# Optimization experiments

Measured on AMD Instinct MI355X. Metric: run time of the kernel, lower is better.

The kernel has to match this reference:

```python
import jax, jax.numpy as jnp
import numpy as np

B = 32            # decode batch (N flat tokens, q_len=1 each)
D_MODEL = 4096
H = 32            # query heads
HKV = 8           # kv heads (GQA)
HD = 128          # head dim
KVLEN = 2048      # context length per sequence
BLOCK = 256       # paged-cache block size
NBPS = KVLEN // BLOCK          # blocks per sequence = 8
NBLOCKS = B * NBPS             # 256
NSLOTS = NBLOCKS * BLOCK       # 65536
EPS = 1e-6
THETA = 10000.0
NEG = -1e30


def setup_inputs() -> dict:
    key = jax.random.key(0)
    ks = jax.random.split(key, 8)
    seqs = jax.random.normal(ks[0], (B, D_MODEL), dtype=jnp.float32)
    Wq = jax.random.normal(ks[1], (D_MODEL, H * HD), dtype=jnp.float32) * 0.02
    Wk = jax.random.normal(ks[2], (D_MODEL, HKV * HD), dtype=jnp.float32) * 0.02
    Wv = jax.random.normal(ks[3], (D_MODEL, HKV * HD), dtype=jnp.float32) * 0.02
    Wo = jax.random.normal(ks[4], (H * HD, D_MODEL), dtype=jnp.float32) * 0.02
    qn_w = jnp.ones((HD,), dtype=jnp.float32)
    kn_w = jnp.ones((HD,), dtype=jnp.float32)
    k_cache = jax.random.normal(ks[5], (NSLOTS, HKV, HD), dtype=jnp.float32) * 0.02
    v_cache = jax.random.normal(ks[6], (NSLOTS, HKV, HD), dtype=jnp.float32) * 0.02
    # decode step: each seq owns NBPS contiguous blocks; new token goes to last slot
    input_pos = jnp.full((B,), KVLEN - 1, dtype=jnp.int32)
    slot_mapping = (jnp.arange(B, dtype=jnp.int32) * NBPS * BLOCK + (KVLEN - 1)).astype(jnp.int32)
    block_tables = jnp.arange(NBLOCKS, dtype=jnp.int32).reshape(B, NBPS)
    context_lens = jnp.full((B,), KVLEN, dtype=jnp.int32)
    return {
        'seqs': seqs, 'Wq': Wq, 'Wk': Wk, 'Wv': Wv, 'Wo': Wo,
        'qn_w': qn_w, 'kn_w': kn_w, 'k_cache': k_cache, 'v_cache': v_cache,
        'input_pos': input_pos, 'slot_mapping': slot_mapping,
        'block_tables': block_tables, 'context_lens': context_lens,
    }


def _rmsnorm(x, w):
    return x * jax.lax.rsqrt(jnp.mean(x * x, axis=-1, keepdims=True) + EPS) * w


def _rope(x, pos):
    # x: [N, heads, HD], pos: [N]
    half = HD // 2
    inv = 1.0 / (THETA ** (jnp.arange(half, dtype=jnp.float32) / half))
    ang = pos.astype(jnp.float32)[:, None] * inv          # [N, half]
    cos = jnp.cos(ang)[:, None, :]
    sin = jnp.sin(ang)[:, None, :]
    x1, x2 = x[..., :half], x[..., half:]
    return jnp.concatenate([x1 * cos - x2 * sin, x2 * cos + x1 * sin], axis=-1)


def reference(seqs, Wq, Wk, Wv, Wo, qn_w, kn_w, k_cache, v_cache,
              input_pos, slot_mapping, block_tables, context_lens):
    # QKV projections (flat token layout, N = B decode tokens)
    q = (seqs @ Wq).reshape(B, H, HD)
    k = (seqs @ Wk).reshape(B, HKV, HD)
    v = (seqs @ Wv).reshape(B, HKV, HD)
    # qk-norm then RoPE
    q = _rmsnorm(q, qn_w)
    k = _rmsnorm(k, kn_w)
    q = _rope(q, input_pos)
    k = _rope(k, input_pos)
    # paged KV-cache store (slot_mapping scatter)
    kc = k_cache.at[slot_mapping].set(k)
    vc = v_cache.at[slot_mapping].set(v)
    # block-table-indexed gather: slots per sequence [B, KVLEN]
    slots = (block_tables[:, :, None] * BLOCK
             + jnp.arange(BLOCK, dtype=jnp.int32)[None, None, :]).reshape(B, -1)
    K = kc[slots]   # [B, L, HKV, HD]
    V = vc[slots]   # [B, L, HKV, HD]
    L = slots.shape[1]
    # GQA attention: group query heads over kv heads
    G = H // HKV
    qg = q.reshape(B, HKV, G, HD)
    scale = 1.0 / jnp.sqrt(jnp.float32(HD))
    scores = jnp.einsum('bkgd,blkd->bkgl', qg, K) * scale   # [B, HKV, G, L]
    valid = jnp.arange(L, dtype=jnp.int32)[None, :] < context_lens[:, None]
    scores = jnp.where(valid[:, None, None, :], scores, NEG)
    p = jax.nn.softmax(scores, axis=-1)
    out = jnp.einsum('bkgl,blkd->bkgd', p, V).reshape(B, H * HD)
    return out @ Wo
```

## Files before the change

kernel.cpp:

```cpp
#include <hip/hip_runtime.h>
#include <hip/hip_bf16.h>
#include <math.h>

#define B_     32
#define DM_    4096
#define H_     32
#define HKV_   8
#define G_     4
#define HD_    128
#define KVLEN_ 2048
#define NBPS_  8
#define NQKV_  6144
#define QKSPLIT_ 32
#define QKC_     128
#define OKSPLIT_ 32
#define OKC_     128
#define ASPLIT_ 16
#define APOS_  128

typedef float vf4 __attribute__((ext_vector_type(4)));
typedef float vf2 __attribute__((ext_vector_type(2)));

__global__ __launch_bounds__(256) void transpose32(
    const float* __restrict__ in, float* __restrict__ out) {
  __shared__ float t[32][65];
  const int tid = threadIdx.x;
  const int k0 = blockIdx.x * 64;
  #pragma unroll
  for (int it = 0; it < 8; ++it) {
    int m = it * 4 + (tid >> 6);
    int k = tid & 63;
    t[m][k] = in[(size_t)m * DM_ + k0 + k];
  }
  __syncthreads();
  #pragma unroll
  for (int it = 0; it < 8; ++it) {
    int flat = it * 256 + tid;
    out[(size_t)k0 * 32 + flat] = t[flat & 31][flat >> 5];
  }
}

__global__ __launch_bounds__(256) void qkv_gemm(
    const float* __restrict__ seqsT, const float* __restrict__ Wq,
    const float* __restrict__ Wk, const float* __restrict__ Wv,
    float* __restrict__ P1) {
  const int tid = threadIdx.x;
  const int nid = blockIdx.x % 24;
  const int kid = blockIdx.x / 24;
  const int k0 = kid * QKC_;

  const int ct = tid & 127;
  const int mh16 = __builtin_amdgcn_readfirstlane((tid >> 7) << 4);
  const int n  = nid * 256 + ct * 2;

  const float* W; int col, ldw;
  if (nid < 16)      { W = Wq; col = n;        ldw = 4096; }
  else if (nid < 20) { W = Wk; col = n - 4096; ldw = 1024; }
  else               { W = Wv; col = n - 5120; ldw = 1024; }

  float2 acc[16];
  #pragma unroll
  for (int r = 0; r < 16; ++r) acc[r] = make_float2(0.f, 0.f);

  const vf2* wp = (const vf2*)(W + (size_t)k0 * ldw + col);
  const int ldw2 = ldw >> 1;
  const vf4* ap = (const vf4*)(seqsT + (size_t)k0 * 32 + mh16);

  #pragma unroll 8
  for (int kk = 0; kk < QKC_; ++kk) {
    vf2 w = __builtin_nontemporal_load(wp + (size_t)kk * ldw2);
    vf4 a0 = ap[kk * 8 + 0];
    vf4 a1 = ap[kk * 8 + 1];
    vf4 a2 = ap[kk * 8 + 2];
    vf4 a3 = ap[kk * 8 + 3];
    #define FMA2(av, r) \
      acc[r].x = fmaf(av, w.x, acc[r].x); acc[r].y = fmaf(av, w.y, acc[r].y);
    FMA2(a0.x, 0)  FMA2(a0.y, 1)  FMA2(a0.z, 2)  FMA2(a0.w, 3)
    FMA2(a1.x, 4)  FMA2(a1.y, 5)  FMA2(a1.z, 6)  FMA2(a1.w, 7)
    FMA2(a2.x, 8)  FMA2(a2.y, 9)  FMA2(a2.z, 10) FMA2(a2.w, 11)
    FMA2(a3.x, 12) FMA2(a3.y, 13) FMA2(a3.z, 14) FMA2(a3.w, 15)
    #undef FMA2
  }

  float* o = P1 + (size_t)kid * 32 * NQKV_ + n;
  #pragma unroll
  for (int r = 0; r < 16; ++r) {
    int m = mh16 + r;
    *(float2*)(o + (size_t)m * NQKV_) = acc[r];
  }
}

__global__ __launch_bounds__(128) void reduce_norm_rope(
    const float* __restrict__ P1, const float* __restrict__ qn_w,
    const float* __restrict__ kn_w, const int* __restrict__ input_pos,
    float* __restrict__ qf, float* __restrict__ knew, float* __restrict__ vnew) {
  const int b = blockIdx.x / 48;
  const int hh = blockIdx.x % 48;
  const int tid = threadIdx.x;

  int col0, kind;
  if (hh < 32)      { kind = 0; col0 = hh * 128; }
  else if (hh < 40) { kind = 1; col0 = 4096 + (hh - 32) * 128; }
  else              { kind = 2; col0 = 5120 + (hh - 40) * 128; }

  float x = 0.f;
  const float* p = P1 + (size_t)b * NQKV_ + col0 + tid;
  #pragma unroll
  for (int s = 0; s < QKSPLIT_; ++s) x += p[(size_t)s * 32 * NQKV_];

  if (kind == 2) {
    vnew[(size_t)b * 1024 + (hh - 40) * 128 + tid] = x;
    return;
  }

  __shared__ float lds[128];
  __shared__ float wred[2];
  float ss = x * x;
  #pragma unroll
  for (int off = 32; off > 0; off >>= 1) ss += __shfl_down(ss, off);
  if ((tid & 63) == 0) wred[tid >> 6] = ss;
  __syncthreads();
  float tot = wred[0] + wred[1];
  float r = rsqrtf(tot * (1.f / 128.f) + 1e-6f);
  const float* wv = (kind == 0) ? qn_w : kn_w;
  x = x * r * wv[tid];

  lds[tid] = x;
  __syncthreads();

  if (tid < 64) {
    float pos = (float)input_pos[b];
    float inv = exp2f(-(float)tid * 0.20762050593045952f);
    float ang = pos * inv;
    float c = cosf(ang), s = sinf(ang);
    float x1 = lds[tid], x2 = lds[tid + 64];
    float o1 = x1 * c - x2 * s;
    float o2 = x2 * c + x1 * s;
    float* dst = (kind == 0) ? (qf + (size_t)b * 4096 + hh * 128)
                             : (knew + (size_t)b * 1024 + (hh - 32) * 128);
    dst[tid] = o1;
    dst[tid + 64] = o2;
  }
}

__global__ __launch_bounds__(512, 4) void attn_decode(
    const float* __restrict__ qf, const float* __restrict__ knew,
    const float* __restrict__ vnew, const float* __restrict__ kc,
    const float* __restrict__ vc, const int* __restrict__ block_tables,
    const int* __restrict__ slot_mapping, const int* __restrict__ context_lens,
    float* __restrict__ pacc, float* __restrict__ pls) {
  const int b   = blockIdx.x >> 4;
  const int sp  = blockIdx.x & 15;
  const int tid = threadIdx.x;
  const int w   = tid >> 6;
  const int lane = tid & 63;
  const int gi  = lane >> 4;
  const int l16 = lane & 15;
  const int d0  = l16 * 8;

  const int ctx   = context_lens[b];
  const int fslot = slot_mapping[b];
  const int base  = sp * APOS_;

  const int page  = block_tables[b * NBPS_ + (base >> 8)];
  const int slot0 = (page << 8) + (base & 255);
  const int rel   = fslot - slot0;
  const bool hasf = (rel >= 0) && (rel < APOS_);
  const int nv    = min(APOS_, ctx - base);

  const float scale = 0.08838834764831845f;
  float q[4][8];
  #pragma unroll
  for (int g = 0; g < 4; ++g) {
    const float4* qp = (const float4*)(qf + ((size_t)b * H_ + w * G_ + g) * HD_ + d0);
    float4 a = qp[0], c = qp[1];
    q[g][0] = a.x * scale; q[g][1] = a.y * scale; q[g][2] = a.z * scale; q[g][3] = a.w * scale;
    q[g][4] = c.x * scale; q[g][5] = c.y * scale; q[g][6] = c.z * scale; q[g][7] = c.w * scale;
  }

  const float* knp = knew + ((size_t)b * HKV_ + w) * HD_ + d0;
  const float* vnp = vnew + ((size_t)b * HKV_ + w) * HD_ + d0;
  const float* kcb = kc + ((size_t)slot0 * HKV_ + w) * HD_ + d0;
  const float* vcb = vc + ((size_t)slot0 * HKV_ + w) * HD_ + d0;

  float ls[4] = {0.f, 0.f, 0.f, 0.f};
  float acc[4][8];
  #pragma unroll
  for (int g = 0; g < 4; ++g)
    #pragma unroll
    for (int j = 0; j < 8; ++j) acc[g][j] = 0.f;

  #define ATTN_STEP(K1, K2, V1, V2, SGN)                                  \
    {                                                                     \
      float kk8[8] = {K1.x, K1.y, K1.z, K1.w, K2.x, K2.y, K2.z, K2.w};    \
      float vv[8]  = {V1.x, V1.y, V1.z, V1.w, V2.x, V2.y, V2.z, V2.w};    \
      float s[4];                                                         \
      _Pragma("unroll")                                                   \
      for (int g = 0; g < 4; ++g) {                                       \
        float t = 0.f;                                                    \
        _Pragma("unroll")                                                 \
        for (int j = 0; j < 8; ++j) t = fmaf(q[g][j], kk8[j], t);         \
        s[g] = t;                                                         \
      }                                                                   \
      _Pragma("unroll")                                                   \
      for (int o2 = 1; o2 < 16; o2 <<= 1) {                               \
        _Pragma("unroll")                                                 \
        for (int g = 0; g < 4; ++g) s[g] += __shfl_xor(s[g], o2);         \
      }                                                                   \
      _Pragma("unroll")                                                   \
      for (int g = 0; g < 4; ++g) {                                       \
        float pw = (SGN) * __expf(s[g]);                                  \
        ls[g] += pw;                                                      \
        _Pragma("unroll")                                                 \
        for (int j = 0; j < 8; ++j) acc[g][j] = fmaf(pw, vv[j], acc[g][j]); \
      }                                                                   \
    }

  if (nv == APOS_) {
    #pragma unroll 2
    for (int it = 0; it < APOS_ / 4; ++it) {
      const int off = it * 4 + gi;
      const vf4* kp4 = (const vf4*)(kcb + (size_t)off * (HKV_ * HD_));
      const vf4* vp4 = (const vf4*)(vcb + (size_t)off * (HKV_ * HD_));
      vf4 k1 = __builtin_nontemporal_load(kp4);
      vf4 k2 = __builtin_nontemporal_load(kp4 + 1);
      vf4 v1 = __builtin_nontemporal_load(vp4);
      vf4 v2 = __builtin_nontemporal_load(vp4 + 1);
      ATTN_STEP(k1, k2, v1, v2, 1.f)
    }
    if (hasf && gi == (rel & 3)) {
      const float* kps = kcb + (size_t)rel * (HKV_ * HD_);
      const float* vps = vcb + (size_t)rel * (HKV_ * HD_);
      float4 k1 = ((const float4*)kps)[0];
      float4 k2 = ((const float4*)kps)[1];
      float4 v1 = ((const float4*)vps)[0];
      float4 v2 = ((const float4*)vps)[1];
      ATTN_STEP(k1, k2, v1, v2, -1.f)
      float4 f1 = ((const float4*)knp)[0];
      float4 f2 = ((const float4*)knp)[1];
      float4 g1 = ((const float4*)vnp)[0];
      float4 g2 = ((const float4*)vnp)[1];
      ATTN_STEP(f1, f2, g1, g2, 1.f)
    }
  } else {
    for (int it = 0; it < APOS_ / 4; ++it) {
      const int off = it * 4 + gi;
      if (base + off < ctx) {
        const float* kp = (off == rel) ? knp : (kcb + (size_t)off * (HKV_ * HD_));
        const float* vp = (off == rel) ? vnp : (vcb + (size_t)off * (HKV_ * HD_));
        float4 k1 = ((const float4*)kp)[0];
        float4 k2 = ((const float4*)kp)[1];
        float4 v1 = ((const float4*)vp)[0];
        float4 v2 = ((const float4*)vp)[1];
        ATTN_STEP(k1, k2, v1, v2, 1.f)
      }
    }
  }
  #undef ATTN_STEP

  #pragma unroll
  for (int o2 = 16; o2 < 64; o2 <<= 1) {
    #pragma unroll
    for (int g = 0; g < 4; ++g) {
      ls[g] += __shfl_xor(ls[g], o2);
      #pragma unroll
      for (int j = 0; j < 8; ++j) acc[g][j] += __shfl_xor(acc[g][j], o2);
    }
  }

  if (gi == 0) {
    #pragma unroll
    for (int g = 0; g < 4; ++g) {
      float* dst = pacc + (((size_t)sp * B_ + b) * H_ + (w * G_ + g)) * HD_ + d0;
      float4 o1 = {acc[g][0], acc[g][1], acc[g][2], acc[g][3]};
      float4 o2 = {acc[g][4], acc[g][5], acc[g][6], acc[g][7]};
      ((float4*)dst)[0] = o1;
      ((float4*)dst)[1] = o2;
      if (l16 == 0) pls[((size_t)sp * B_ + b) * H_ + (w * G_ + g)] = ls[g];
    }
  }
}

__global__ __launch_bounds__(256) void attn_mergeT(
    const float* __restrict__ pacc, const float* __restrict__ pls,
    float* __restrict__ attnT) {
  const int idx = blockIdx.x * 256 + threadIdx.x;
  const int b   = idx >> 10;
  const int h   = (idx >> 5) & 31;
  const int d4  = (idx & 31) * 4;
  const int bh  = idx >> 5;
  const float4* p4 = (const float4*)pacc;
  float4 A = {0.f, 0.f, 0.f, 0.f};
  float L = 0.f;
  #pragma unroll
  for (int sp = 0; sp < ASPLIT_; ++sp) {
    float4 t = p4[(size_t)sp * 32768 + idx];
    A.x += t.x; A.y += t.y; A.z += t.z; A.w += t.w;
    L += pls[sp * (B_ * H_) + bh];
  }
  float r = 1.f / L;
  float* dst = attnT + ((size_t)(h * 128 + d4)) * 32 + b;
  dst[0]  = A.x * r;
  dst[32] = A.y * r;
  dst[64] = A.z * r;
  dst[96] = A.w * r;
}

__global__ __launch_bounds__(256) void oproj_gemm(
    const float* __restrict__ attnT, const float* __restrict__ Wo,
    float* __restrict__ P2) {
  const int tid = threadIdx.x;
  const int nid = blockIdx.x & 15;
  const int kid = blockIdx.x >> 4;
  const int k0 = kid * OKC_;

  const int ct = tid & 127;
  const int mh16 = __builtin_amdgcn_readfirstlane((tid >> 7) << 4);
  const int n  = nid * 256 + ct * 2;

  float2 acc[16];
  #pragma unroll
  for (int r = 0; r < 16; ++r) acc[r] = make_float2(0.f, 0.f);

  const vf2* wp = (const vf2*)(Wo + (size_t)k0 * 4096 + n);
  const vf4* ap = (const vf4*)(attnT + (size_t)k0 * 32 + mh16);

  #pragma unroll 8
  for (int kk = 0; kk < OKC_; ++kk) {
    vf2 w = __builtin_nontemporal_load(wp + (size_t)kk * 2048);
    vf4 a0 = ap[kk * 8 + 0];
    vf4 a1 = ap[kk * 8 + 1];
    vf4 a2 = ap[kk * 8 + 2];
    vf4 a3 = ap[kk * 8 + 3];
    #define FMA2(av, r) \
      acc[r].x = fmaf(av, w.x, acc[r].x); acc[r].y = fmaf(av, w.y, acc[r].y);
    FMA2(a0.x, 0)  FMA2(a0.y, 1)  FMA2(a0.z, 2)  FMA2(a0.w, 3)
    FMA2(a1.x, 4)  FMA2(a1.y, 5)  FMA2(a1.z, 6)  FMA2(a1.w, 7)
    FMA2(a2.x, 8)  FMA2(a2.y, 9)  FMA2(a2.z, 10) FMA2(a2.w, 11)
    FMA2(a3.x, 12) FMA2(a3.y, 13) FMA2(a3.z, 14) FMA2(a3.w, 15)
    #undef FMA2
  }

  float* o = P2 + (size_t)kid * 32 * 4096 + n;
  #pragma unroll
  for (int r = 0; r < 16; ++r) {
    int m = mh16 + r;
    *(float2*)(o + (size_t)m * 4096) = acc[r];
  }
}

__global__ __launch_bounds__(256) void oproj_reduce(
    const float* __restrict__ P2, float* __restrict__ out) {
  const int idx = blockIdx.x * 256 + threadIdx.x;
  const float4* p4 = (const float4*)P2;
  float4 s = {0.f, 0.f, 0.f, 0.f};
  #pragma unroll
  for (int t = 0; t < OKSPLIT_; ++t) {
    float4 v = p4[(size_t)t * 32768 + idx];
    s.x += v.x; s.y += v.y; s.z += v.z; s.w += v.w;
  }
  ((float4*)out)[idx] = s;
}

extern "C" void kernel_launch(void* const* d_in, const int* in_sizes, int n_in,
                              void* d_out, int out_size, void* d_ws, size_t ws_size,
                              hipStream_t stream) {
  const float* seqs = (const float*)d_in[0];
  const float* Wq   = (const float*)d_in[1];
  const float* Wk   = (const float*)d_in[2];
  const float* Wv   = (const float*)d_in[3];
  const float* Wo   = (const float*)d_in[4];
  const float* qn_w = (const float*)d_in[5];
  const float* kn_w = (const float*)d_in[6];
  const float* kc   = (const float*)d_in[7];
  const float* vc   = (const float*)d_in[8];
  const int* input_pos = (const int*)d_in[9];
  const int* slot_map  = (const int*)d_in[10];
  const int* btab      = (const int*)d_in[11];
  const int* ctx       = (const int*)d_in[12];
  float* out = (float*)d_out;

  char* w = (char*)d_ws;
  float* seqsT = (float*)(w);
  float* P1    = (float*)(w + 524288);
  float* qf    = (float*)(w + 25690112);
  float* knew  = (float*)(w + 26214400);
  float* vnew  = (float*)(w + 26345472);
  float* attnT = (float*)(w + 26476544);
  float* pacc  = (float*)(w + 27000832);
  float* pls   = (float*)(w + 35389440);
  float* P2    = (float*)(w + 35454976);

  transpose32<<<64, 256, 0, stream>>>(seqs, seqsT);
  qkv_gemm<<<24 * QKSPLIT_, 256, 0, stream>>>(seqsT, Wq, Wk, Wv, P1);
  reduce_norm_rope<<<B_ * 48, 128, 0, stream>>>(P1, qn_w, kn_w, input_pos, qf, knew, vnew);
  attn_decode<<<B_ * ASPLIT_, 512, 0, stream>>>(qf, knew, vnew, kc, vc, btab, slot_map, ctx, pacc, pls);
  attn_mergeT<<<128, 256, 0, stream>>>(pacc, pls, attnT);
  oproj_gemm<<<16 * OKSPLIT_, 256, 0, stream>>>(attnT, Wo, P2);
  oproj_reduce<<<128, 256, 0, stream>>>(P2, out);
}
```

Before: 186.8 us.

## Stage KV cache through LDS with double-buffered global_load_lds in attention

The full-block path of the decode attention kernel now loads K and V through direct global-to-LDS loads into a per-wave double buffer. The next iteration's tile is prefetched while the current one is read from LDS, with explicit vmcnt waits. The goal is to hide memory latency and keep more loads in flight than the previous register nontemporal loads did. In exchange it uses 64KB of shared memory per block, which may limit occupancy under launch_bounds(512,4), and it adds an LDS round trip. The loop is also no longer unrolled.

```diff
diff --git a/kernel.cpp b/kernel.cpp
--- a/kernel.cpp
+++ b/kernel.cpp
@@ -21,6 +21,12 @@
 typedef float vf4 __attribute__((ext_vector_type(4)));
 typedef float vf2 __attribute__((ext_vector_type(2)));
 
+__device__ __forceinline__ void gl_lds(const float* g, float* l) {
+  __builtin_amdgcn_global_load_lds(
+      (const __attribute__((address_space(1))) void*)g,
+      (__attribute__((address_space(3))) void*)l, 16, 0, 0);
+}
+
 __global__ __launch_bounds__(256) void transpose32(
     const float* __restrict__ in, float* __restrict__ out) {
   __shared__ float t[32][65];
@@ -149,6 +155,7 @@
     const float* __restrict__ vc, const int* __restrict__ block_tables,
     const int* __restrict__ slot_mapping, const int* __restrict__ context_lens,
     float* __restrict__ pacc, float* __restrict__ pls) {
+  __shared__ float alds[16384];
   const int b   = blockIdx.x >> 4;
   const int sp  = blockIdx.x & 15;
   const int tid = threadIdx.x;
@@ -182,6 +189,12 @@
   const float* vnp = vnew + ((size_t)b * HKV_ + w) * HD_ + d0;
   const float* kcb = kc + ((size_t)slot0 * HKV_ + w) * HD_ + d0;
   const float* vcb = vc + ((size_t)slot0 * HKV_ + w) * HD_ + d0;
+
+  const float* ksrc0 = kc + (size_t)slot0 * 1024 + (size_t)(lane >> 5) * 1024
+                          + w * 128 + (lane & 31) * 4;
+  const float* vsrc0 = vc + (size_t)slot0 * 1024 + (size_t)(lane >> 5) * 1024
+                          + w * 128 + (lane & 31) * 4;
+  const int wofs = __builtin_amdgcn_readfirstlane(w * 2048);
 
   float ls[4] = {0.f, 0.f, 0.f, 0.f};
   float acc[4][8];
@@ -217,17 +230,35 @@
     }
 
   if (nv == APOS_) {
-    #pragma unroll 2
-    for (int it = 0; it < APOS_ / 4; ++it) {
-      const int off = it * 4 + gi;
-      const vf4* kp4 = (const vf4*)(kcb + (size_t)off * (HKV_ * HD_));
-      const vf4* vp4 = (const vf4*)(vcb + (size_t)off * (HKV_ * HD_));
-      vf4 k1 = __builtin_nontemporal_load(kp4);
-      vf4 k2 = __builtin_nontemporal_load(kp4 + 1);
-      vf4 v1 = __builtin_nontemporal_load(vp4);
-      vf4 v2 = __builtin_nontemporal_load(vp4 + 1);
+    #define STAGE(T, BF) {                                                \
+      const float* ks_ = ksrc0 + (size_t)(T) * 4096;                      \
+      const float* vs_ = vsrc0 + (size_t)(T) * 4096;                      \
+      float* lk_ = &alds[wofs + (BF) * 1024];                             \
+      float* lv_ = lk_ + 512;                                             \
+      gl_lds(ks_, lk_);                                                   \
+      gl_lds(ks_ + 2048, lk_ + 256);                                      \
+      gl_lds(vs_, lv_);                                                   \
+      gl_lds(vs_ + 2048, lv_ + 256);                                      \
+    }
+    STAGE(0, 0)
+    #pragma unroll 1
+    for (int t = 0; t < APOS_ / 4; ++t) {
+      const int bf = t & 1;
+      if (t + 1 < APOS_ / 4) {
+        STAGE(t + 1, bf ^ 1)
+        asm volatile("s_waitcnt vmcnt(4)" ::: "memory");
+      } else {
+        asm volatile("s_waitcnt vmcnt(0)" ::: "memory");
+      }
+      __builtin_amdgcn_sched_barrier(0);
+      const vf4* lk4 = (const vf4*)&alds[wofs + bf * 1024 + gi * 128 + d0];
+      const vf4* lv4 = (const vf4*)&alds[wofs + bf * 1024 + 512 + gi * 128 + d0];
+      vf4 k1 = lk4[0], k2 = lk4[1];
+      vf4 v1 = lv4[0], v2 = lv4[1];
       ATTN_STEP(k1, k2, v1, v2, 1.f)
     }
+    #undef STAGE
+
     if (hasf && gi == (rel & 3)) {
       const float* kps = kcb + (size_t)rel * (HKV_ * HD_);
       const float* vps = vcb + (size_t)rel * (HKV_ * HD_);
```

Measured after the change: 204.6 us. +9.5%, slower.
